# Optimization experiments

Measured on AMD Instinct MI355X. Metric: run time of the kernel, lower is better.

The kernel has to match this reference:

```python
import jax, jax.numpy as jnp
import numpy as np

DILATION = (1, 1)


def pd_indexing2d(x, dh, dw, dilation):
    """Pitch-dependent indexing. x:(B,C,H,W); dh,dw:(B,1,W) -> list of 9 (B,C,H,W)."""
    B, C, H, W = x.shape
    # dilation factors, clamped to >= 1, broadcast to (B,1,1,W)
    dil_h = jnp.maximum((dh * dilation[0]).astype(jnp.int32), 1)[:, :, None, :]
    dil_w = jnp.maximum((dw * dilation[1]).astype(jnp.int32), 1)[:, :, None, :]

    rH = jnp.arange(H)[None, None, :, None]   # (1,1,H,1)
    cW = jnp.arange(W)[None, None, None, :]   # (1,1,1,W)

    # row (frequency) indices
    idxD = jnp.abs(rH - dil_h) % H            # (B,1,H,W)
    up = rH + dil_h
    idxU = jnp.where(up >= H, rH, up)         # overflow -> idxU - dil = base
    rows = [idxD, jnp.broadcast_to(rH, (1, 1, H, 1)), idxU]

    # col (time) indices
    idxL = jnp.abs(cW - dil_w) % W            # (B,1,1,W)
    rt = cW + dil_w
    # torch uses negative index -(rt % W) - 1 == W - 1 - (rt % W)
    idxR = jnp.where(rt >= W, W - 1 - (rt % W), rt)
    cols = [idxL, jnp.broadcast_to(cW, (1, 1, 1, W)), idxR]

    bidx = jnp.arange(B).reshape(B, 1, 1, 1)
    cidx = jnp.arange(C).reshape(1, C, 1, 1)
    xs = []
    for r in rows:
        for c in cols:
            xs.append(x[bidx, cidx, r, c])
    return xs


def setup_inputs() -> dict:
    key = jax.random.key(0)
    k1, k2, k3, k4, k5 = jax.random.split(key, 5)
    B, C, O, H, W = 8, 64, 64, 80, 800
    x = jax.random.normal(k1, (B, C, H, W), dtype=jnp.float32)
    dh = jax.random.randint(k2, (B, 1, W), 1, 4).astype(jnp.float32)
    dw = jax.random.randint(k3, (B, 1, W), 1, 4).astype(jnp.float32)
    weight = jax.random.normal(k4, (9, O, C), dtype=jnp.float32) * 0.05
    bias = jax.random.normal(k5, (O,), dtype=jnp.float32) * 0.05
    return {"x": x, "dh": dh, "dw": dw, "weight": weight, "bias": bias}


def reference(x, dh, dw, weight, bias):
    xs = pd_indexing2d(x, dh, dw, DILATION)
    out = jnp.einsum('bchw,oc->bohw', xs[0], weight[0]) + bias[None, :, None, None]
    for k in range(1, 9):
        out = out + jnp.einsum('bchw,oc->bohw', xs[k], weight[k])
    return out
```

## Files before the change

kernel.cpp:

```cpp
#include <hip/hip_runtime.h>

#define B_  8
#define C_  64
#define O_  64
#define H_  80
#define W_  800
#define NCHT   13
#define NCHM   25
#define XT_BYTES 65536000u

#define ROWS_ 8
#define ROWB_ 5120
#define LDSX_BYTES (ROWS_ * ROWB_ + 1024)

typedef short bf16x8 __attribute__((ext_vector_type(8)));
typedef float f32x4  __attribute__((ext_vector_type(4)));

__device__ __forceinline__ unsigned short f2bf(float f) {
    unsigned int u = __float_as_uint(f);
    unsigned int r = u + 0x7FFFu + ((u >> 16) & 1u);
    return (unsigned short)(r >> 16);
}

__device__ __forceinline__ void gld_lds16(const void* g, void* l) {
    __builtin_amdgcn_global_load_lds(
        (const __attribute__((address_space(1))) unsigned int*)g,
        (__attribute__((address_space(3))) unsigned int*)l, 16, 0, 0);
}

__global__ void k_transpose(const float* __restrict__ x, unsigned short* __restrict__ xT) {
    __shared__ float tile[64][68];
    const int chunk = blockIdx.x, h = blockIdx.y, b = blockIdx.z;
    const int w0 = chunk * 64;
    const int tid = threadIdx.x;

    const int wf4 = tid & 15;
    const int c0  = tid >> 4;
    const int w   = w0 + wf4 * 4;
#pragma unroll
    for (int it = 0; it < 4; ++it) {
        const int c = it * 16 + c0;
        f32x4 v = {0.f, 0.f, 0.f, 0.f};
        if (w < W_) v = *(const f32x4*)(x + (((b * C_ + c) * H_ + h) * W_) + w);
        *(f32x4*)&tile[c][wf4 * 4] = v;
    }
    __syncthreads();

    const int px = tid >> 2, q = tid & 3;
    const int wabs = w0 + px;
    if (wabs < W_) {
        unsigned int u[8];
#pragma unroll
        for (int i = 0; i < 8; ++i) {
            const int c = q * 16 + 2 * i;
            u[i] = (unsigned int)f2bf(tile[c][px])
                 | ((unsigned int)f2bf(tile[c + 1][px]) << 16);
        }
        unsigned int* base = (unsigned int*)xT + ((size_t)((b * H_ + h) * W_) + wabs) * 32;
        const int g0 = (2 * q + wabs) & 7;
        const int g1 = (2 * q + 1 + wabs) & 7;
        *(uint4*)(base + g0 * 4) = make_uint4(u[0], u[1], u[2], u[3]);
        *(uint4*)(base + g1 * 4) = make_uint4(u[4], u[5], u[6], u[7]);
    }
}

__global__ void k_wfrag(const float* __restrict__ wt, unsigned short* __restrict__ wf) {
    const int t = blockIdx.x * 256 + threadIdx.x;
    const int j    = t & 7;
    const int lane = (t >> 3) & 63;
    const int mt   = (t >> 9) & 3;
    const int ks   = t >> 11;
    const int tap  = ks >> 1, hf = ks & 1;
    const int o = mt * 16 + (lane & 15);
    const int c = hf * 32 + (lane >> 4) * 8 + j;
    wf[t] = f2bf(wt[(tap * 64 + o) * 64 + c]);
}

__global__ void __launch_bounds__(256, 3)
k_main(const unsigned short* __restrict__ xT,
       const unsigned short* __restrict__ wfrag,
       const float* __restrict__ dh, const float* __restrict__ dw,
       const float* __restrict__ bias, float* __restrict__ out) {
    __shared__ char lx[LDSX_BYTES];
    const int tid  = threadIdx.x;
    const int wave = tid >> 6, lane = tid & 63;

    const unsigned int flat = blockIdx.x;
    const int b = flat & 7;
    const unsigned int l = flat >> 3;
    const int chunk = l % NCHM;
    const int hp    = l / NCHM;
    const int h0 = hp * 2;
    const int w0 = chunk * 32;
    const int h   = h0 + (wave & 1);
    const int mtb = (wave >> 1) * 2;
    const int l15 = lane & 15, kq = lane >> 4;

    {
        const int col0  = (w0 - 3) < 0 ? 0 : (w0 - 3);
        const int shift = (col0 - (w0 - 3)) * 128;
#pragma unroll
        for (int k = 0; k < 2; ++k) {
            const int slot = wave * 2 + k;
            int ar = h0 - 3 + slot;
            ar = ar < 0 ? 0 : (ar > H_ - 1 ? H_ - 1 : ar);
            const char* src = (const char*)xT
                + ((size_t)(b * H_ + ar) * W_ + col0) * 128;
            char* dst = lx + slot * ROWB_ + shift;
#pragma unroll
            for (int i = 0; i < 5; ++i)
                gld_lds16(src + i * 1024 + lane * 16, dst + i * 1024);
        }
    }

    unsigned int rowb[2][3], colb[2][3];
#pragma unroll
    for (int nt = 0; nt < 2; ++nt) {
        const int pw  = w0 + nt * 16 + l15;
        const int dhi = (int)dh[b * W_ + pw];
        const int dwi = (int)dw[b * W_ + pw];
        int rD = h - dhi;   if (rD < 0) rD = -rD;
        const int rU = (h + dhi < H_) ? (h + dhi) : h;
        int cL = pw - dwi;  if (cL < 0) cL = -cL;
        const int cR = (pw + dwi < W_) ? (pw + dwi) : (2 * W_ - 1 - pw - dwi);
        rowb[nt][0] = (unsigned int)(rD - h0 + 3) * ROWB_;
        rowb[nt][1] = (unsigned int)(h  - h0 + 3) * ROWB_;
        rowb[nt][2] = (unsigned int)(rU - h0 + 3) * ROWB_;
        const int cs[3] = {cL, pw, cR};
#pragma unroll
        for (int j = 0; j < 3; ++j)
            colb[nt][j] = (unsigned int)(cs[j] - (w0 - 3)) * 128u
                        + (unsigned int)(((cs[j] + kq) & 7) * 16);
    }

    const char* wfb = (const char*)wfrag;
    const unsigned int aoff = (unsigned int)lane * 16u;

    f32x4 acc[2][2];
#pragma unroll
    for (int mtl = 0; mtl < 2; ++mtl) {
        const f32x4 bv = *(const f32x4*)(bias + (mtb + mtl) * 16 + kq * 4);
#pragma unroll
        for (int nt = 0; nt < 2; ++nt)
#pragma unroll
            for (int r = 0; r < 4; ++r) acc[mtl][nt][r] = bv[r];
    }

    __syncthreads();

    bf16x8 bcur[2], bnxt[2], a0[2], a1[2], a2[2];
#pragma unroll
    for (int nt = 0; nt < 2; ++nt)
        bcur[nt] = *(const bf16x8*)(lx + rowb[nt][0] + colb[nt][0]);
#pragma unroll
    for (int mtl = 0; mtl < 2; ++mtl) {
        a0[mtl] = *(const bf16x8*)(wfb + (unsigned int)((0 * 4 + mtb + mtl) * 1024) + aoff);
        a1[mtl] = *(const bf16x8*)(wfb + (unsigned int)((1 * 4 + mtb + mtl) * 1024) + aoff);
    }

#pragma unroll
    for (int s = 0; s < 18; ++s) {
        if (s < 17) {
            const int sn = s + 1;
            const int tap = sn >> 1, hf = sn & 1;
            const int i = tap / 3, j = tap % 3;
#pragma unroll
            for (int nt = 0; nt < 2; ++nt) {
                unsigned int a = rowb[nt][i] + colb[nt][j];
                if (hf) a ^= 64u;
                bnxt[nt] = *(const bf16x8*)(lx + a);
            }
        }
        if (s < 16) {
#pragma unroll
            for (int mtl = 0; mtl < 2; ++mtl)
                a2[mtl] = *(const bf16x8*)(wfb
                            + (unsigned int)(((s + 2) * 4 + mtb + mtl) * 1024) + aoff);
        }
#pragma unroll
        for (int mtl = 0; mtl < 2; ++mtl)
#pragma unroll
            for (int nt = 0; nt < 2; ++nt)
                acc[mtl][nt] = __builtin_amdgcn_mfma_f32_16x16x32_bf16(
                    a0[mtl], bcur[nt], acc[mtl][nt], 0, 0, 0);
#pragma unroll
        for (int nt = 0; nt < 2; ++nt) bcur[nt] = bnxt[nt];
#pragma unroll
        for (int mtl = 0; mtl < 2; ++mtl) { a0[mtl] = a1[mtl]; a1[mtl] = a2[mtl]; }
    }

#pragma unroll
    for (int mtl = 0; mtl < 2; ++mtl) {
#pragma unroll
        for (int nt = 0; nt < 2; ++nt) {
            const int w = w0 + nt * 16 + l15;
            const unsigned int ob =
                ((unsigned int)(b * O_ + (mtb + mtl) * 16 + kq * 4) * (unsigned int)H_
                 + (unsigned int)h) * (unsigned int)W_ + (unsigned int)w;
#pragma unroll
            for (int r = 0; r < 4; ++r)
                out[ob + (unsigned int)r * 64000u] = acc[mtl][nt][r];
        }
    }
}

extern "C" void kernel_launch(void* const* d_in, const int* in_sizes, int n_in,
                              void* d_out, int out_size, void* d_ws, size_t ws_size,
                              hipStream_t stream) {
    const float* x      = (const float*)d_in[0];
    const float* dh     = (const float*)d_in[1];
    const float* dw     = (const float*)d_in[2];
    const float* weight = (const float*)d_in[3];
    const float* bias   = (const float*)d_in[4];
    float* out = (float*)d_out;

    unsigned short* xT    = (unsigned short*)d_ws;
    unsigned short* wfrag = (unsigned short*)((char*)d_ws + XT_BYTES);

    k_transpose<<<dim3(NCHT, H_, B_), 256, 0, stream>>>(x, xT);
    k_wfrag<<<dim3(144), 256, 0, stream>>>(weight, wfrag);
    k_main<<<dim3(NCHM * (H_ / 2) * B_), 256, 0, stream>>>(xT, wfrag, dh, dw, bias, out);
}
```

Baseline: 292.8 us.

## Process four rows per 512-thread block and fuse weight prep into transpose

The main kernel now uses 512-thread blocks that cover four output rows instead of two. Each block stages a 10-row halo in LDS rather than 8 rows per two output rows, which cuts redundant global-to-LDS loads of neighbouring rows. The weight-fragment conversion moves into extra blocks of the transpose kernel, removing one launch. The transpose's second phase also remaps threads so each wave handles one channel group while lanes walk pixels, which changes both the LDS read pattern and the global store pattern. The cost is larger per-block LDS and larger blocks, which may limit how many blocks fit on a CU.

```diff
diff --git a/kernel.cpp b/kernel.cpp
--- a/kernel.cpp
+++ b/kernel.cpp
@@ -9,7 +9,7 @@
 #define NCHM   25
 #define XT_BYTES 65536000u
 
-#define ROWS_ 8
+#define ROWS_ 10
 #define ROWB_ 5120
 #define LDSX_BYTES (ROWS_ * ROWB_ + 1024)
 
@@ -28,11 +28,29 @@
         (__attribute__((address_space(3))) unsigned int*)l, 16, 0, 0);
 }
 
-__global__ void k_transpose(const float* __restrict__ x, unsigned short* __restrict__ xT) {
+__global__ void k_prep(const float* __restrict__ x, const float* __restrict__ wt,
+                       unsigned short* __restrict__ xT, unsigned short* __restrict__ wf) {
     __shared__ float tile[64][68];
+    const int tid = threadIdx.x;
+
+    if (blockIdx.y >= H_) {
+        const int idx = ((int)(blockIdx.y - H_) * B_ + (int)blockIdx.z) * NCHT + (int)blockIdx.x;
+        const int t = idx * 256 + tid;
+        if (t < 36864) {
+            const int j    = t & 7;
+            const int lane = (t >> 3) & 63;
+            const int mt   = (t >> 9) & 3;
+            const int ks   = t >> 11;
+            const int tap  = ks >> 1, hf = ks & 1;
+            const int o = mt * 16 + (lane & 15);
+            const int c = hf * 32 + (lane >> 4) * 8 + j;
+            wf[t] = f2bf(wt[(tap * 64 + o) * 64 + c]);
+        }
+        return;
+    }
+
     const int chunk = blockIdx.x, h = blockIdx.y, b = blockIdx.z;
     const int w0 = chunk * 64;
-    const int tid = threadIdx.x;
 
     const int wf4 = tid & 15;
     const int c0  = tid >> 4;
@@ -46,37 +64,25 @@
     }
     __syncthreads();
 
-    const int px = tid >> 2, q = tid & 3;
+    const int wv = tid >> 6, px = tid & 63;
     const int wabs = w0 + px;
     if (wabs < W_) {
         unsigned int u[8];
 #pragma unroll
         for (int i = 0; i < 8; ++i) {
-            const int c = q * 16 + 2 * i;
+            const int c = wv * 16 + 2 * i;
             u[i] = (unsigned int)f2bf(tile[c][px])
                  | ((unsigned int)f2bf(tile[c + 1][px]) << 16);
         }
         unsigned int* base = (unsigned int*)xT + ((size_t)((b * H_ + h) * W_) + wabs) * 32;
-        const int g0 = (2 * q + wabs) & 7;
-        const int g1 = (2 * q + 1 + wabs) & 7;
+        const int g0 = (2 * wv + wabs) & 7;
+        const int g1 = (2 * wv + 1 + wabs) & 7;
         *(uint4*)(base + g0 * 4) = make_uint4(u[0], u[1], u[2], u[3]);
         *(uint4*)(base + g1 * 4) = make_uint4(u[4], u[5], u[6], u[7]);
     }
 }
 
-__global__ void k_wfrag(const float* __restrict__ wt, unsigned short* __restrict__ wf) {
-    const int t = blockIdx.x * 256 + threadIdx.x;
-    const int j    = t & 7;
-    const int lane = (t >> 3) & 63;
-    const int mt   = (t >> 9) & 3;
-    const int ks   = t >> 11;
-    const int tap  = ks >> 1, hf = ks & 1;
-    const int o = mt * 16 + (lane & 15);
-    const int c = hf * 32 + (lane >> 4) * 8 + j;
-    wf[t] = f2bf(wt[(tap * 64 + o) * 64 + c]);
-}
-
-__global__ void __launch_bounds__(256, 3)
+__global__ void __launch_bounds__(512, 6)
 k_main(const unsigned short* __restrict__ xT,
        const unsigned short* __restrict__ wfrag,
        const float* __restrict__ dh, const float* __restrict__ dw,
@@ -89,11 +95,11 @@
     const int b = flat & 7;
     const unsigned int l = flat >> 3;
     const int chunk = l % NCHM;
-    const int hp    = l / NCHM;
-    const int h0 = hp * 2;
+    const int hq    = l / NCHM;
+    const int h0 = hq * 4;
     const int w0 = chunk * 32;
-    const int h   = h0 + (wave & 1);
-    const int mtb = (wave >> 1) * 2;
+    const int h   = h0 + (wave & 3);
+    const int mtb = (wave >> 2) * 2;
     const int l15 = lane & 15, kq = lane >> 4;
 
     {
@@ -101,15 +107,17 @@
         const int shift = (col0 - (w0 - 3)) * 128;
 #pragma unroll
         for (int k = 0; k < 2; ++k) {
-            const int slot = wave * 2 + k;
-            int ar = h0 - 3 + slot;
-            ar = ar < 0 ? 0 : (ar > H_ - 1 ? H_ - 1 : ar);
-            const char* src = (const char*)xT
-                + ((size_t)(b * H_ + ar) * W_ + col0) * 128;
-            char* dst = lx + slot * ROWB_ + shift;
-#pragma unroll
-            for (int i = 0; i < 5; ++i)
-                gld_lds16(src + i * 1024 + lane * 16, dst + i * 1024);
+            const int slot = wave + k * 8;
+            if (slot < ROWS_) {
+                int ar = h0 - 3 + slot;
+                ar = ar < 0 ? 0 : (ar > H_ - 1 ? H_ - 1 : ar);
+                const char* src = (const char*)xT
+                    + ((size_t)(b * H_ + ar) * W_ + col0) * 128;
+                char* dst = lx + slot * ROWB_ + shift;
+#pragma unroll
+                for (int i = 0; i < 5; ++i)
+                    gld_lds16(src + i * 1024 + lane * 16, dst + i * 1024);
+            }
         }
     }
 
@@ -217,7 +225,6 @@
     unsigned short* xT    = (unsigned short*)d_ws;
     unsigned short* wfrag = (unsigned short*)((char*)d_ws + XT_BYTES);
 
-    k_transpose<<<dim3(NCHT, H_, B_), 256, 0, stream>>>(x, xT);
-    k_wfrag<<<dim3(144), 256, 0, stream>>>(weight, wfrag);
-    k_main<<<dim3(NCHM * (H_ / 2) * B_), 256, 0, stream>>>(xT, wfrag, dh, dw, bias, out);
-}
+    k_prep<<<dim3(NCHT, H_ + 2, B_), 256, 0, stream>>>(x, weight, xT, wfrag);
+    k_main<<<dim3(NCHM * (H_ / 4) * B_), 512, 0, stream>>>(xT, wfrag, dh, dw, bias, out);
+}
```

New measurement: 310.3 us. 1.06x slower.

## Fuse transpose/bf16 conversion into main kernel, enlarge tile to four rows

Applied to the files above, without the earlier changes.

Drops the separate transpose kernel that wrote a bf16 channel-last copy of x to workspace. The main kernel now reads fp32 x directly, converts it to bf16 and writes the swizzled layout into LDS. Blocks grow to 512 threads covering four output rows, so each block loads 10 halo rows instead of 8 for 2 rows. This removes an extra global write and read of x. In exchange, the main kernel now does strided per-channel global loads (8 channels per lane, each 256 KB apart) and does the conversion in-kernel.

```diff
diff --git a/kernel.cpp b/kernel.cpp
--- a/kernel.cpp
+++ b/kernel.cpp
@@ -5,13 +5,12 @@
 #define O_  64
 #define H_  80
 #define W_  800
-#define NCHT   13
 #define NCHM   25
-#define XT_BYTES 65536000u
 
-#define ROWS_ 8
-#define ROWB_ 5120
-#define LDSX_BYTES (ROWS_ * ROWB_ + 1024)
+#define ROWS_  10
+#define ROWPX_ 40
+#define ROWB_  (ROWPX_ * 128)
+#define LDSX_BYTES (ROWS_ * ROWB_)
 
 typedef short bf16x8 __attribute__((ext_vector_type(8)));
 typedef float f32x4  __attribute__((ext_vector_type(4)));
@@ -20,48 +19,6 @@
     unsigned int u = __float_as_uint(f);
     unsigned int r = u + 0x7FFFu + ((u >> 16) & 1u);
     return (unsigned short)(r >> 16);
-}
-
-__device__ __forceinline__ void gld_lds16(const void* g, void* l) {
-    __builtin_amdgcn_global_load_lds(
-        (const __attribute__((address_space(1))) unsigned int*)g,
-        (__attribute__((address_space(3))) unsigned int*)l, 16, 0, 0);
-}
-
-__global__ void k_transpose(const float* __restrict__ x, unsigned short* __restrict__ xT) {
-    __shared__ float tile[64][68];
-    const int chunk = blockIdx.x, h = blockIdx.y, b = blockIdx.z;
-    const int w0 = chunk * 64;
-    const int tid = threadIdx.x;
-
-    const int wf4 = tid & 15;
-    const int c0  = tid >> 4;
-    const int w   = w0 + wf4 * 4;
-#pragma unroll
-    for (int it = 0; it < 4; ++it) {
-        const int c = it * 16 + c0;
-        f32x4 v = {0.f, 0.f, 0.f, 0.f};
-        if (w < W_) v = *(const f32x4*)(x + (((b * C_ + c) * H_ + h) * W_) + w);
-        *(f32x4*)&tile[c][wf4 * 4] = v;
-    }
-    __syncthreads();
-
-    const int px = tid >> 2, q = tid & 3;
-    const int wabs = w0 + px;
-    if (wabs < W_) {
-        unsigned int u[8];
-#pragma unroll
-        for (int i = 0; i < 8; ++i) {
-            const int c = q * 16 + 2 * i;
-            u[i] = (unsigned int)f2bf(tile[c][px])
-                 | ((unsigned int)f2bf(tile[c + 1][px]) << 16);
-        }
-        unsigned int* base = (unsigned int*)xT + ((size_t)((b * H_ + h) * W_) + wabs) * 32;
-        const int g0 = (2 * q + wabs) & 7;
-        const int g1 = (2 * q + 1 + wabs) & 7;
-        *(uint4*)(base + g0 * 4) = make_uint4(u[0], u[1], u[2], u[3]);
-        *(uint4*)(base + g1 * 4) = make_uint4(u[4], u[5], u[6], u[7]);
-    }
 }
 
 __global__ void k_wfrag(const float* __restrict__ wt, unsigned short* __restrict__ wf) {
@@ -76,8 +33,8 @@
     wf[t] = f2bf(wt[(tap * 64 + o) * 64 + c]);
 }
 
-__global__ void __launch_bounds__(256, 3)
-k_main(const unsigned short* __restrict__ xT,
+__global__ void __launch_bounds__(512, 4)
+k_main(const float* __restrict__ x,
        const unsigned short* __restrict__ wfrag,
        const float* __restrict__ dh, const float* __restrict__ dw,
        const float* __restrict__ bias, float* __restrict__ out) {
@@ -89,27 +46,36 @@
     const int b = flat & 7;
     const unsigned int l = flat >> 3;
     const int chunk = l % NCHM;
-    const int hp    = l / NCHM;
-    const int h0 = hp * 2;
+    const int hq    = l / NCHM;
+    const int h0 = hq * 4;
     const int w0 = chunk * 32;
-    const int h   = h0 + (wave & 1);
-    const int mtb = (wave >> 1) * 2;
+    const int h   = h0 + (wave & 3);
+    const int mtb = (wave >> 2) * 2;
     const int l15 = lane & 15, kq = lane >> 4;
 
     {
-        const int col0  = (w0 - 3) < 0 ? 0 : (w0 - 3);
-        const int shift = (col0 - (w0 - 3)) * 128;
+        const int colabs = w0 - 3 + lane;
+        if (lane < ROWPX_ && colabs >= 0 && colabs < W_) {
 #pragma unroll
-        for (int k = 0; k < 2; ++k) {
-            const int slot = wave * 2 + k;
-            int ar = h0 - 3 + slot;
-            ar = ar < 0 ? 0 : (ar > H_ - 1 ? H_ - 1 : ar);
-            const char* src = (const char*)xT
-                + ((size_t)(b * H_ + ar) * W_ + col0) * 128;
-            char* dst = lx + slot * ROWB_ + shift;
+            for (int t = 0; t < 10; ++t) {
+                const int task = wave * 10 + t;
+                const int row = task >> 3, g = task & 7;
+                int ar = h0 - 3 + row;
+                ar = ar < 0 ? 0 : (ar > H_ - 1 ? H_ - 1 : ar);
+                const float* src = x + ((size_t)(b * C_ + g * 8) * H_ + ar) * W_ + colabs;
+                float v[8];
 #pragma unroll
-            for (int i = 0; i < 5; ++i)
-                gld_lds16(src + i * 1024 + lane * 16, dst + i * 1024);
+                for (int c = 0; c < 8; ++c) v[c] = src[(size_t)c * (H_ * W_)];
+                unsigned int u[4];
+#pragma unroll
+                for (int i = 0; i < 4; ++i)
+                    u[i] = (unsigned int)f2bf(v[2 * i])
+                         | ((unsigned int)f2bf(v[2 * i + 1]) << 16);
+                char* dst = lx + (unsigned int)row * (unsigned int)ROWB_
+                          + (unsigned int)lane * 128u
+                          + (unsigned int)(((g + colabs) & 7) * 16);
+                *(uint4*)dst = make_uint4(u[0], u[1], u[2], u[3]);
+            }
         }
     }
 
@@ -214,10 +180,8 @@
     const float* bias   = (const float*)d_in[4];
     float* out = (float*)d_out;
 
-    unsigned short* xT    = (unsigned short*)d_ws;
-    unsigned short* wfrag = (unsigned short*)((char*)d_ws + XT_BYTES);
+    unsigned short* wfrag = (unsigned short*)d_ws;
 
-    k_transpose<<<dim3(NCHT, H_, B_), 256, 0, stream>>>(x, xT);
     k_wfrag<<<dim3(144), 256, 0, stream>>>(weight, wfrag);
-    k_main<<<dim3(NCHM * (H_ / 2) * B_), 256, 0, stream>>>(xT, wfrag, dh, dw, bias, out);
+    k_main<<<dim3(NCHM * (H_ / 4) * B_), 512, 0, stream>>>(x, wfrag, dh, dw, bias, out);
 }
```

Measured after the change: 307.8 us. 5.1% more time.
